# Performance work log

Hardware: AMD Instinct MI355X
Metric: run time of the kernel (lower is better)

## Reference

```python
import jax, jax.numpy as jnp
import numpy as np

SPIRAL_LEN = 12
V_LEVELS = [32768, 8192, 2048, 512, 128]
CHANNELS = [3, 32, 64, 128, 256]


def spiral_conv(x, spiral, W, b):
    # x: [B, V, C_in]; spiral: [V, S] neighbor indices
    B, V, C = x.shape
    g = x[:, spiral, :]                      # [B, V, S, C_in] irregular gather
    g = g.reshape(B, V, -1)                  # [B, V, S*C_in]
    return g @ W + b                         # [B, V, C_out]


def mesh_pool(x, idx, w):
    # sparse down_transform (<=3 nnz per row): out[b,i,:] = sum_k w[i,k] * x[b, idx[i,k], :]
    return jnp.einsum('bvkc,vk->bvc', x[:, idx, :], w)


def setup_inputs() -> dict:
    key = jax.random.key(0)
    ks = jax.random.split(key, 32)
    S = SPIRAL_LEN
    V = V_LEVELS
    C = CHANNELS
    d = {}
    d['x'] = jax.random.normal(ks[0], (32, V[0], C[0]), dtype=jnp.float32)
    for i in range(4):
        d[f'spiral{i}'] = jax.random.randint(ks[1 + i], (V[i], S), 0, V[i])
        d[f'didx{i}'] = jax.random.randint(ks[5 + i], (V[i + 1], 3), 0, V[i])
        w = jax.random.uniform(ks[9 + i], (V[i + 1], 3), dtype=jnp.float32)
        d[f'dw{i}'] = w / w.sum(-1, keepdims=True)  # barycentric-like rows
        fan_in = S * C[i]
        d[f'W{i}'] = jax.random.normal(ks[13 + i], (fan_in, C[i + 1]), dtype=jnp.float32) * np.float32(1.0 / np.sqrt(fan_in))
        d[f'b{i}'] = jnp.zeros((C[i + 1],), jnp.float32)
    flat_in = V[4] * C[4]  # num_vert * out_channels[-2]
    d['Wl1'] = jax.random.normal(ks[20], (flat_in, 512), dtype=jnp.float32) * np.float32(1.0 / np.sqrt(flat_in))
    d['bl1'] = jnp.zeros((512,), jnp.float32)
    d['Wl2'] = jax.random.normal(ks[21], (512, 64), dtype=jnp.float32) * np.float32(1.0 / np.sqrt(512))
    d['bl2'] = jnp.zeros((64,), jnp.float32)
    return d


def reference(x, spiral0, spiral1, spiral2, spiral3,
              didx0, didx1, didx2, didx3,
              dw0, dw1, dw2, dw3,
              W0, b0, W1, b1, W2, b2, W3, b3,
              Wl1, bl1, Wl2, bl2):
    spirals = (spiral0, spiral1, spiral2, spiral3)
    didx = (didx0, didx1, didx2, didx3)
    dw = (dw0, dw1, dw2, dw3)
    Wb = ((W0, b0), (W1, b1), (W2, b2), (W3, b3))
    for i in range(4):  # SpiralEnblock: elu(spiral_conv(x)) -> sparse pool
        x = jax.nn.elu(spiral_conv(x, spirals[i], *Wb[i]))
        x = mesh_pool(x, didx[i], dw[i])
    B = x.shape[0]
    x = x.reshape(B, -1)                     # [B, num_vert * C_last]
    x = jax.nn.elu(x @ Wl1 + bl1)            # [B, 512]
    y = x @ Wl2 + bl2                        # [B, latent]
    return (x, y)
```

## Files before the change

### kernel.cpp

```cpp
#include <hip/hip_runtime.h>
#include <cstdint>
#include <cstddef>

typedef _Float16 f16x8 __attribute__((ext_vector_type(8)));
typedef _Float16 f16x4 __attribute__((ext_vector_type(4)));
typedef float f32x4 __attribute__((ext_vector_type(4)));

static __device__ __forceinline__ float elu_f(float t) {
    return t > 0.0f ? t : expm1f(t);
}

typedef __attribute__((address_space(1))) const unsigned int guint;
typedef __attribute__((address_space(3))) unsigned int       luint;
static __device__ __forceinline__ void gload_lds16(const void* g, void* l)
{
    __builtin_amdgcn_global_load_lds((guint*)g, (luint*)l, 16, 0, 0);
}

template<int N>
static __device__ __forceinline__ void vm_wait()
{
    static_assert(N == 0 || N == 4 || N == 5, "vmcnt literal");
    if constexpr (N == 0)      asm volatile("s_waitcnt vmcnt(0)" ::: "memory");
    else if constexpr (N == 4) asm volatile("s_waitcnt vmcnt(4)" ::: "memory");
    else                       asm volatile("s_waitcnt vmcnt(5)" ::: "memory");
    __builtin_amdgcn_sched_barrier(0);
}

static __device__ __forceinline__ int block_pu0(int bid, int P, int vshift_out, int nbl)
{
    if (nbl < 0) return bid * P;
    int xcd  = bid & 7;
    int slot = bid >> 3;
    int nb   = slot & ((1 << nbl) - 1);
    int tile = slot >> nbl;
    return ((xcd + (nb << 3)) << vshift_out) + tile * P;
}

template<int KTOT, int C_OUT, int BN>
static __device__ __forceinline__ void prep_w_body(const float* __restrict__ W,
                                                   _Float16* __restrict__ o, int i)
{
    constexpr int KT = KTOT/64;
    int j = i & 7;
    int rest = i >> 3;
    int n = rest % BN;
    int kc = (rest / BN) & 7;
    int t = (rest / (BN*8)) % KT;
    int y = rest / (BN*8*KT);
    int k = t*64 + kc*8 + j;
    o[i] = (_Float16)W[(size_t)k*C_OUT + y*BN + n];
}

__global__ __launch_bounds__(256)
void setup_all(const float* __restrict__ x0, _Float16* __restrict__ xT,
               const float* __restrict__ W0, const float* __restrict__ W1,
               const float* __restrict__ W2, const float* __restrict__ W3,
               const int* __restrict__ didx0, const int* __restrict__ spiral0,
               _Float16* __restrict__ w0h, _Float16* __restrict__ w1h,
               _Float16* __restrict__ w2h, _Float16* __restrict__ w3h,
               unsigned int* __restrict__ g)
{
    __shared__ _Float16 t[16][64*4 + 8];
    const int tid = threadIdx.x;
    int bid = blockIdx.x;

    if (bid < 1024) {
        const int h  = bid >> 9;
        const float* x = x0 + (size_t)h*16*98304;
        _Float16* xTh  = xT + (size_t)h*2097152;
        const int v0 = (bid & 511) * 64;
        #pragma unroll
        for (int it = 0; it < 4; ++it) {
            int e = it*256 + tid;
            int b = e >> 6, v = e & 63;
            const float* p = x + ((size_t)b*32768 + v0 + v)*3;
            f16x4 hh;
            hh[0] = (_Float16)p[0]; hh[1] = (_Float16)p[1];
            hh[2] = (_Float16)p[2]; hh[3] = (_Float16)0.f;
            *(f16x4*)&t[b][v*4] = hh;
        }
        __syncthreads();
        #pragma unroll
        for (int it = 0; it < 2; ++it) {
            int e = it*256 + tid;
            int vl = e >> 3, s = e & 7;
            f16x4 a = *(const f16x4*)&t[2*s][vl*4];
            f16x4 b = *(const f16x4*)&t[2*s+1][vl*4];
            f16x8 hh;
            hh[0]=a[0]; hh[1]=a[1]; hh[2]=a[2]; hh[3]=a[3];
            hh[4]=b[0]; hh[5]=b[1]; hh[6]=b[2]; hh[7]=b[3];
            *(f16x8*)&xTh[((size_t)(v0+vl)*16 + s*2)*4] = hh;
        }
        return;
    }
    bid -= 1024;

    if (bid < 8) {
        int i = bid*256 + tid;
        int j = i & 7;
        int n = (i >> 3) & 31;
        int kc = i >> 8;
        int k = kc*8 + j;
        int s = k >> 2, c = k & 3;
        float v = (s < 12 && c < 3) ? W0[(size_t)(s*3 + c)*32 + n] : 0.0f;
        w0h[i] = (_Float16)v;
    } else if (bid < 104) {
        prep_w_body< 384,  64, 64>(W1, w1h, (bid - 8)*256 + tid);
    } else if (bid < 488) {
        prep_w_body< 768, 128, 64>(W2, w2h, (bid - 104)*256 + tid);
    } else if (bid < 2024) {
        prep_w_body<1536, 256, 64>(W3, w3h, (bid - 488)*256 + tid);
    } else {
        int i = (bid - 2024)*256 + tid;
        int q = i & 7;
        int row = i >> 3;
        unsigned int val = 0;
        if (q < 6) {
            int v = didx0[row];
            unsigned int s0 = (unsigned int)spiral0[v*12 + q*2];
            unsigned int s1 = (unsigned int)spiral0[v*12 + q*2 + 1];
            val = s0 | (s1 << 16);
        }
        g[i] = val;
    }
}

__global__ __launch_bounds__(256)
void conv0T(const _Float16* __restrict__ xT0, const unsigned int* __restrict__ gidx,
            const _Float16* __restrict__ Wp, const float* __restrict__ bias,
            const float* __restrict__ dwt, _Float16* __restrict__ out0)
{
    __shared__ _Float16 Ep[4][512];
    const int h = blockIdx.x >> 10;
    const _Float16* xT = xT0 + (size_t)h*2097152;
    _Float16* out = out0 + (size_t)h*16*262144;
    const int tid  = threadIdx.x;
    const int wave = tid >> 6;
    const int lane = tid & 63;
    const int quad = lane >> 4;
    const int l16  = lane & 15;
    const int u0   = (blockIdx.x & 1023) * 8 + wave * 2;

    f16x8 bf[2][2];
    #pragma unroll
    for (int kt = 0; kt < 2; ++kt)
        #pragma unroll
        for (int nt = 0; nt < 2; ++nt)
            bf[kt][nt] = *(const f16x8*)&Wp[(((kt*4+quad)*32) + nt*16 + l16)*8];
    float bv[2] = { bias[l16], bias[16 + l16] };

    #pragma unroll
    for (int ui = 0; ui < 2; ++ui) {
        int u = u0 + ui;
        f32x4 pacc[2] = {{0.f,0.f,0.f,0.f},{0.f,0.f,0.f,0.f}};
        #pragma unroll
        for (int kp = 0; kp < 3; ++kp) {
            int r = u*3 + kp;
            unsigned int gp0 = gidx[r*8 + quad];
            unsigned int gp1 = gidx[r*8 + 4 + quad];
            f16x4 a0 = *(const f16x4*)&xT[(size_t)(gp0 & 0xffffu)*64 + l16*4];
            f16x4 a1 = *(const f16x4*)&xT[(size_t)(gp0 >> 16)*64 + l16*4];
            f16x4 a2 = *(const f16x4*)&xT[(size_t)(gp1 & 0xffffu)*64 + l16*4];
            f16x4 a3 = *(const f16x4*)&xT[(size_t)(gp1 >> 16)*64 + l16*4];
            f16x8 af0, af1;
            af0[0]=a0[0]; af0[1]=a0[1]; af0[2]=a0[2]; af0[3]=a0[3];
            af0[4]=a1[0]; af0[5]=a1[1]; af0[6]=a1[2]; af0[7]=a1[3];
            af1[0]=a2[0]; af1[1]=a2[1]; af1[2]=a2[2]; af1[3]=a2[3];
            af1[4]=a3[0]; af1[5]=a3[1]; af1[6]=a3[2]; af1[7]=a3[3];
            float dw = dwt[r];
            #pragma unroll
            for (int nt = 0; nt < 2; ++nt) {
                f32x4 m = {0.f,0.f,0.f,0.f};
                m = __builtin_amdgcn_mfma_f32_16x16x32_f16(af0, bf[0][nt], m, 0,0,0);
                m = __builtin_amdgcn_mfma_f32_16x16x32_f16(af1, bf[1][nt], m, 0,0,0);
                #pragma unroll
                for (int rr = 0; rr < 4; ++rr)
                    pacc[nt][rr] += dw * elu_f(m[rr] + bv[nt]);
            }
        }
        #pragma unroll
        for (int nt = 0; nt < 2; ++nt)
            #pragma unroll
            for (int rr = 0; rr < 4; ++rr)
                Ep[wave][(quad*4+rr)*32 + nt*16 + l16] = (_Float16)pacc[nt][rr];
        int b  = lane >> 2;
        int c8 = lane & 3;
        f16x8 rowv = *(const f16x8*)&Ep[wave][b*32 + c8*8];
        *(f16x8*)&out[(size_t)b*262144 + (size_t)u*32 + c8*8] = rowv;
    }
}

template<int C_IN, int C_OUT, int P, int BN, int WGM, int WGN, bool OUT_HALF, int NBUF>
__global__ __launch_bounds__(256)
void conv_pool_mfma(const _Float16* __restrict__ x, const int* __restrict__ spiral,
                    const _Float16* __restrict__ Wp, const float* __restrict__ bias,
                    const int* __restrict__ didx, const float* __restrict__ dwt,
                    void* __restrict__ outv, int vshift_in, int vshift_out, int nbl)
{
    constexpr int R    = 3*P;
    constexpr int KTOT = 12*C_IN;
    constexpr int KT   = KTOT/64;
    constexpr int NST  = KT*2;
    constexpr int WTM  = R/WGM;
    constexpr int WTN  = BN/WGN;
    constexpr int NMT  = WTM/16;
    constexpr int NNT  = WTN/16;
    constexpr int C4   = BN/4;
    constexpr int GS   = (C_IN == 32) ? 1 : 2;
    constexpr int NG   = NST / GS;
    constexpr int CPR  = GS * 4;
    constexpr int CPRS = (CPR == 4) ? 2 : 3;
    constexpr int ACH  = R * CPR;
    constexpr int BCH  = GS * BN * 4;
    constexpr int AIPW = ACH / 256;
    constexpr int BIPW = BCH / 256;
    constexpr int LPW  = AIPW + BIPW;
    constexpr int ASUBH = R * GS * 32;
    constexpr int BSUBH = GS * 32 * BN;
    static_assert(WTM % 16 == 0 && WTN % 16 == 0, "tile");
    static_assert(R <= 256 && (P*C4) % 256 == 0, "loops");
    static_assert(ACH % 256 == 0 && BCH % 256 == 0, "stage");
    static_assert(NST % GS == 0 && GS*32 <= C_IN, "group");
    static_assert(NBUF == 2 || NBUF == 3, "nbuf");
    static_assert(NBUF == 2 ? NG >= 2 : NG >= 3, "pipeline depth");

    constexpr size_t BUFB = (size_t)(NBUF*(ASUBH + BSUBH)) * 2;
    constexpr size_t EB   = (size_t)R * (BN + 4) * 2;
    constexpr size_t GOFF = (BUFB > EB ? BUFB : EB);
    static_assert(GOFF + (size_t)R*12*2 <= 65536, "LDS budget");
    __shared__ __align__(16) char smem[GOFF + (size_t)R*12*2];
    _Float16* Ab = (_Float16*)smem;
    _Float16* Bb = (_Float16*)(smem + (size_t)NBUF*ASUBH*2);
    unsigned short* gidx = (unsigned short*)(smem + GOFF);
    _Float16* E = (_Float16*)smem;

    const int tid  = threadIdx.x;
    const int wave = tid >> 6;
    const int lane = tid & 63;
    const int quad = lane >> 4;
    const int l16  = lane & 15;
    const int wm   = wave / WGN;
    const int wn   = wave % WGN;
    const int pu0  = block_pu0(blockIdx.x, P, vshift_out, nbl);
    const int n0   = blockIdx.y * BN;
    const int vmask_out = (1 << vshift_out) - 1;
    const int base_in = (pu0 >> vshift_out) << vshift_in;

    if (tid < R) {
        int ul = tid / 3;
        int kp = tid - ul*3;
        int u  = (pu0 + ul) & vmask_out;
        int v  = didx[u*3 + kp];
        const int* svp = spiral + v*12;
        #pragma unroll
        for (int j = 0; j < 12; ++j) gidx[tid*12 + j] = (unsigned short)svp[j];
    }
    __syncthreads();

    f32x4 acc[NMT][NNT];
    #pragma unroll
    for (int i = 0; i < NMT; ++i)
        #pragma unroll
        for (int j = 0; j < NNT; ++j) acc[i][j] = (f32x4){0.f, 0.f, 0.f, 0.f};

    const _Float16* xb = x + (size_t)base_in * C_IN;

    auto SWZ = [](int r) -> int {
        return (CPR == 4) ? ((r & 3) ^ ((r >> 2) & 3)) : (r & 7);
    };

    auto stage = [&](int g, int buf) {
        const int k0g = g * GS * 32;
        const int sv  = k0g / C_IN;
        const int c0  = k0g % C_IN;
        _Float16* Ad = Ab + (size_t)buf * ASUBH;
        #pragma unroll
        for (int i = 0; i < AIPW; ++i) {
            int t  = (wave*AIPW + i)*64 + lane;
            int r  = t >> CPRS;
            int q  = t & (CPR - 1);
            int qq = q ^ SWZ(r);
            int gr = gidx[r*12 + sv];
            gload_lds16(xb + (size_t)gr*C_IN + c0 + qq*8,
                        Ad + (size_t)(wave*AIPW + i)*512);
        }
        _Float16* Bd = Bb + (size_t)buf * BSUBH;
        const _Float16* bs = Wp + ((size_t)(blockIdx.y*NST + g*GS)*4)*BN*8;
        #pragma unroll
        for (int i = 0; i < BIPW; ++i) {
            int t = (wave*BIPW + i)*64 + lane;
            gload_lds16(bs + (size_t)t*8,
                        Bd + (size_t)(wave*BIPW + i)*512);
        }
    };

    auto compute = [&](int cb) {
        const _Float16* Ar = Ab + (size_t)cb * ASUBH;
        const _Float16* Br = Bb + (size_t)cb * BSUBH;
        #pragma unroll
        for (int sl = 0; sl < GS; ++sl) {
            f16x8 af[NMT], bf[NNT];
            #pragma unroll
            for (int i = 0; i < NMT; ++i) {
                int m = wm*WTM + i*16 + l16;
                af[i] = *(const f16x8*)&Ar[(size_t)(m*CPR + ((sl*4 + quad) ^ SWZ(m)))*8];
            }
            #pragma unroll
            for (int j = 0; j < NNT; ++j) {
                int n = wn*WTN + j*16 + l16;
                bf[j] = *(const f16x8*)&Br[(size_t)((sl*4 + quad)*BN + n)*8];
            }
            #pragma unroll
            for (int i = 0; i < NMT; ++i)
                #pragma unroll
                for (int j = 0; j < NNT; ++j)
                    acc[i][j] = __builtin_amdgcn_mfma_f32_16x16x32_f16(
                        af[i], bf[j], acc[i][j], 0, 0, 0);
        }
    };

    if constexpr (NBUF == 3) {
        stage(0, 0);
        stage(1, 1);
        int cur = 0;
        for (int g = 0; g < NG; ++g) {
            if (g + 1 < NG) vm_wait<LPW>(); else vm_wait<0>();
            __builtin_amdgcn_s_barrier();
            __builtin_amdgcn_sched_barrier(0);
            int nx2 = cur + 2; if (nx2 >= 3) nx2 -= 3;
            if (g + 2 < NG) stage(g + 2, nx2);
            compute(cur);
            asm volatile("s_waitcnt lgkmcnt(0)" ::: "memory");
            __builtin_amdgcn_sched_barrier(0);
            __builtin_amdgcn_s_barrier();
            __builtin_amdgcn_sched_barrier(0);
            cur = (cur + 1 == 3) ? 0 : cur + 1;
        }
    } else {
        stage(0, 0);
        int cur = 0;
        for (int g = 0; g < NG; ++g) {
            if (g + 1 < NG) {
                stage(g + 1, cur ^ 1);
                vm_wait<LPW>();
            } else {
                vm_wait<0>();
            }
            __builtin_amdgcn_s_barrier();
            __builtin_amdgcn_sched_barrier(0);
            compute(cur);
            asm volatile("s_waitcnt lgkmcnt(0)" ::: "memory");
            __builtin_amdgcn_sched_barrier(0);
            __builtin_amdgcn_s_barrier();
            __builtin_amdgcn_sched_barrier(0);
            cur ^= 1;
        }
    }

    float bv[NNT];
    #pragma unroll
    for (int j = 0; j < NNT; ++j)
        bv[j] = bias[n0 + wn*WTN + j*16 + l16];

    #pragma unroll
    for (int i = 0; i < NMT; ++i) {
        int row_base = wm*WTM + i*16 + quad*4;
        #pragma unroll
        for (int j = 0; j < NNT; ++j) {
            int col = wn*WTN + j*16 + l16;
            #pragma unroll
            for (int r = 0; r < 4; ++r)
                E[(size_t)(row_base + r)*(BN+4) + col] =
                    (_Float16)elu_f(acc[i][j][r] + bv[j]);
        }
    }
    __syncthreads();

    #pragma unroll
    for (int e = tid; e < P*C4; e += 256) {
        int ul = e / C4;
        int c4 = e - ul*C4;
        int pu = pu0 + ul;
        int u  = pu & vmask_out;
        const float* w = dwt + u*3;
        f16x4 a0 = *(const f16x4*)&E[(size_t)(ul*3 + 0)*(BN+4) + c4*4];
        f16x4 a1 = *(const f16x4*)&E[(size_t)(ul*3 + 1)*(BN+4) + c4*4];
        f16x4 a2 = *(const f16x4*)&E[(size_t)(ul*3 + 2)*(BN+4) + c4*4];
        float ox = w[0]*(float)a0[0] + w[1]*(float)a1[0] + w[2]*(float)a2[0];
        float oy = w[0]*(float)a0[1] + w[1]*(float)a1[1] + w[2]*(float)a2[1];
        float oz = w[0]*(float)a0[2] + w[1]*(float)a1[2] + w[2]*(float)a2[2];
        float ow = w[0]*(float)a0[3] + w[1]*(float)a1[3] + w[2]*(float)a2[3];
        if (OUT_HALF) {
            f16x4 h; h[0]=(_Float16)ox; h[1]=(_Float16)oy; h[2]=(_Float16)oz; h[3]=(_Float16)ow;
            *(f16x4*)&((_Float16*)outv)[(size_t)pu*C_OUT + n0 + c4*4] = h;
        } else {
            float4 o; o.x=ox; o.y=oy; o.z=oz; o.w=ow;
            *(float4*)&((float*)outv)[(size_t)pu*C_OUT + n0 + c4*4] = o;
        }
    }
}

__global__ __launch_bounds__(256)
void fc1_partial(const float* __restrict__ xflat, const float* __restrict__ Wl1,
                 float* __restrict__ partial)
{
    __shared__ float sb[8704];
    const int tid = threadIdx.x;
    const int n4 = tid & 31;
    const int kq = (tid >> 5) & 3;
    const int mh = tid >> 7;
    const int nt = blockIdx.x;
    const int ks = blockIdx.y;
    const int kbase = ks * 128;

    for (int e = tid; e < 1024; e += 256) {
        int m = e >> 5, k4 = e & 31;
        *(float4*)&sb[m*128 + k4*4] = *(const float4*)&xflat[(size_t)m*32768 + kbase + k4*4];
    }
    __syncthreads();

    float acc[16][4];
    #pragma unroll
    for (int m = 0; m < 16; ++m)
        #pragma unroll
        for (int c = 0; c < 4; ++c) acc[m][c] = 0.0f;

    const float* Wb = Wl1 + (size_t)(kbase + kq*32)*512 + nt*128 + n4*4;
    #pragma unroll 2
    for (int i = 0; i < 32; i += 4) {
        float4 w0 = *(const float4*)(Wb + (size_t)(i+0)*512);
        float4 w1 = *(const float4*)(Wb + (size_t)(i+1)*512);
        float4 w2 = *(const float4*)(Wb + (size_t)(i+2)*512);
        float4 w3 = *(const float4*)(Wb + (size_t)(i+3)*512);
        #pragma unroll
        for (int m = 0; m < 16; ++m) {
            float4 xv = *(const float4*)&sb[(mh*16 + m)*128 + kq*32 + i];
            acc[m][0] += xv.x*w0.x + xv.y*w1.x + xv.z*w2.x + xv.w*w3.x;
            acc[m][1] += xv.x*w0.y + xv.y*w1.y + xv.z*w2.y + xv.w*w3.y;
            acc[m][2] += xv.x*w0.z + xv.y*w1.z + xv.z*w2.z + xv.w*w3.z;
            acc[m][3] += xv.x*w0.w + xv.y*w1.w + xv.z*w2.w + xv.w*w3.w;
        }
    }
    __syncthreads();

    int slot = (mh*2 + (kq >> 1))*32 + n4;
    if (kq & 1) {
        #pragma unroll
        for (int m = 0; m < 16; ++m)
            *(float4*)&sb[slot*68 + m*4] = *(float4*)&acc[m][0];
    }
    __syncthreads();
    if (!(kq & 1)) {
        #pragma unroll
        for (int m = 0; m < 16; ++m) {
            float4 v = *(const float4*)&sb[slot*68 + m*4];
            acc[m][0] += v.x; acc[m][1] += v.y; acc[m][2] += v.z; acc[m][3] += v.w;
        }
    }
    __syncthreads();
    int slot2 = mh*32 + n4;
    if (kq == 2) {
        #pragma unroll
        for (int m = 0; m < 16; ++m)
            *(float4*)&sb[slot2*68 + m*4] = *(float4*)&acc[m][0];
    }
    __syncthreads();
    if (kq == 0) {
        float* pb = partial + ((size_t)(ks*4 + nt)*32 + mh*16)*128 + n4*4;
        #pragma unroll
        for (int m = 0; m < 16; ++m) {
            float4 v = *(const float4*)&sb[slot2*68 + m*4];
            float4 o;
            o.x = acc[m][0] + v.x; o.y = acc[m][1] + v.y;
            o.z = acc[m][2] + v.z; o.w = acc[m][3] + v.w;
            *(float4*)(pb + (size_t)m*128) = o;
        }
    }
}

__global__ __launch_bounds__(512)
void fc1_finish(const float* __restrict__ partial, const float* __restrict__ bl1,
                const float* __restrict__ Wl2, const float* __restrict__ bl2,
                float* __restrict__ out)
{
    __shared__ float hh[512];
    __shared__ float ps[512];
    const int m = blockIdx.x;
    const int tid = threadIdx.x;
    const int nt = tid >> 7, nl = tid & 127;

    const float* p = partial + ((size_t)nt*32 + m)*128 + nl;
    float s = 0.0f;
    #pragma unroll 8
    for (int ks = 0; ks < 256; ++ks)
        s += p[(size_t)ks*16384];
    float h = elu_f(s + bl1[tid]);
    out[(size_t)m*512 + tid] = h;
    hh[tid] = h;
    __syncthreads();

    const int c  = tid & 63;
    const int kc = tid >> 6;
    float a = 0.0f;
    #pragma unroll 8
    for (int k = kc*64; k < kc*64 + 64; ++k)
        a += hh[k] * Wl2[(size_t)k*64 + c];
    ps[tid] = a;
    __syncthreads();
    if (tid < 64) {
        float y = bl2[tid];
        #pragma unroll
        for (int j = 0; j < 8; ++j) y += ps[j*64 + tid];
        out[16384 + (size_t)m*64 + tid] = y;
    }
}

extern "C" void kernel_launch(void* const* d_in, const int* in_sizes, int n_in,
                              void* d_out, int out_size, void* d_ws, size_t ws_size,
                              hipStream_t stream)
{
    (void)in_sizes; (void)n_in; (void)out_size; (void)ws_size;

    const float* x0 = (const float*)d_in[0];
    const int*   sp[4]; const int* didx[4]; const float* dwp[4];
    const float* Wp[4]; const float* bp[4];
    for (int i = 0; i < 4; ++i) {
        sp[i]   = (const int*)  d_in[1 + i*5 + 0];
        didx[i] = (const int*)  d_in[1 + i*5 + 1];
        dwp[i]  = (const float*)d_in[1 + i*5 + 2];
        Wp[i]   = (const float*)d_in[1 + i*5 + 3];
        bp[i]   = (const float*)d_in[1 + i*5 + 4];
    }
    const float* Wl1 = (const float*)d_in[21];
    const float* bl1 = (const float*)d_in[22];
    const float* Wl2 = (const float*)d_in[23];
    const float* bl2 = (const float*)d_in[24];
    float* out = (float*)d_out;

    char* wsb = (char*)d_ws;
    float* persist      = (float*)wsb;
    float* partial      = (float*)(wsb + (4<<20));
    _Float16* xT        = (_Float16*)(wsb + (24<<20));
    _Float16* pooled0   = (_Float16*)(wsb + (32<<20));
    _Float16* pooled1   = (_Float16*)(wsb + (48<<20));
    _Float16* pooled2   = (_Float16*)(wsb + (56<<20));
    unsigned int* gidx0 = (unsigned int*)(wsb + (60<<20));
    _Float16* w0h       = (_Float16*)(wsb + (61<<20));
    _Float16* w1h       = w0h + 2048;
    _Float16* w2h       = w1h + 24576;
    _Float16* w3h       = w2h + 98304;

    setup_all<<<3816, 256, 0, stream>>>(x0, xT,
                                        Wp[0], Wp[1], Wp[2], Wp[3],
                                        didx[0], sp[0],
                                        w0h, w1h, w2h, w3h, gidx0);

    conv0T<<<2048, 256, 0, stream>>>(xT, gidx0, w0h, bp[0], dwp[0], pooled0);

    conv_pool_mfma<32,64,64,64,4,1,true,2><<<1024, 256, 0, stream>>>(
        pooled0, sp[1], w1h, bp[1], didx[1], dwp[1], pooled1, 13, 11, 2);

    conv_pool_mfma<64,128,32,64,2,2,true,3><<<dim3(512, 2), 256, 0, stream>>>(
        pooled1, sp[2], w2h, bp[2], didx[2], dwp[2], pooled2, 11, 9, 2);

    conv_pool_mfma<128,256,32,64,2,2,false,3><<<dim3(128, 4), 256, 0, stream>>>(
        pooled2, sp[3], w3h, bp[3], didx[3], dwp[3], persist, 9, 7, 2);

    fc1_partial<<<dim3(4, 256), 256, 0, stream>>>(persist, Wl1, partial);
    fc1_finish<<<32, 512, 0, stream>>>(partial, bl1, Wl2, bl2, out);
}
```

Measured before the change: 269.2 us.

## Load conv weight fragments directly into registers instead of staging through LDS

Adds a BREG mode to the spiral conv+pool MFMA kernel in which B (weight) fragments are loaded from global memory straight into double-buffered registers, and only the gathered A tile goes through LDS via the triple-buffered global_load_lds path. The main loop is unrolled by two to ping-pong the register buffers, and the vmcnt waits are retuned to cover both A and B loads. This is meant to remove the LDS write/read traffic and footprint for the weights in layers 2 and 3. In exchange each wave issues redundant global loads for B, since the tile is no longer shared through LDS, and register pressure rises.

After: 266.4 us. About the same (-1.1%).

```diff
diff --git a/kernel.cpp b/kernel.cpp
--- a/kernel.cpp
+++ b/kernel.cpp
@@ -20,10 +20,11 @@
 template<int N>
 static __device__ __forceinline__ void vm_wait()
 {
-    static_assert(N == 0 || N == 4 || N == 5, "vmcnt literal");
+    static_assert(N == 0 || N == 4 || N == 5 || N == 7, "vmcnt literal");
     if constexpr (N == 0)      asm volatile("s_waitcnt vmcnt(0)" ::: "memory");
     else if constexpr (N == 4) asm volatile("s_waitcnt vmcnt(4)" ::: "memory");
-    else                       asm volatile("s_waitcnt vmcnt(5)" ::: "memory");
+    else if constexpr (N == 5) asm volatile("s_waitcnt vmcnt(5)" ::: "memory");
+    else                       asm volatile("s_waitcnt vmcnt(7)" ::: "memory");
     __builtin_amdgcn_sched_barrier(0);
 }
 
@@ -191,7 +192,7 @@
     }
 }
 
-template<int C_IN, int C_OUT, int P, int BN, int WGM, int WGN, bool OUT_HALF, int NBUF>
+template<int C_IN, int C_OUT, int P, int BN, int WGM, int WGN, bool OUT_HALF, int NBUF, bool BREG>
 __global__ __launch_bounds__(256)
 void conv_pool_mfma(const _Float16* __restrict__ x, const int* __restrict__ spiral,
                     const _Float16* __restrict__ Wp, const float* __restrict__ bias,
@@ -216,16 +217,21 @@
     constexpr int AIPW = ACH / 256;
     constexpr int BIPW = BCH / 256;
     constexpr int LPW  = AIPW + BIPW;
+    constexpr int NB   = GS * NNT;
+    constexpr int FULLW = AIPW + NB;
     constexpr int ASUBH = R * GS * 32;
     constexpr int BSUBH = GS * 32 * BN;
     static_assert(WTM % 16 == 0 && WTN % 16 == 0, "tile");
     static_assert(R <= 256 && (P*C4) % 256 == 0, "loops");
-    static_assert(ACH % 256 == 0 && BCH % 256 == 0, "stage");
+    static_assert(ACH % 256 == 0, "stageA");
+    static_assert(BREG || BCH % 256 == 0, "stageB");
     static_assert(NST % GS == 0 && GS*32 <= C_IN, "group");
     static_assert(NBUF == 2 || NBUF == 3, "nbuf");
-    static_assert(NBUF == 2 ? NG >= 2 : NG >= 3, "pipeline depth");
-
-    constexpr size_t BUFB = (size_t)(NBUF*(ASUBH + BSUBH)) * 2;
+    static_assert(!BREG || (NBUF == 3 && NG % 2 == 0 && NG >= 4), "breg pipeline");
+    static_assert(BREG || (NBUF == 2 ? NG >= 2 : NG >= 3), "pipeline depth");
+
+    constexpr size_t BUFB = (BREG ? (size_t)NBUF*ASUBH
+                                  : (size_t)NBUF*(ASUBH + BSUBH)) * 2;
     constexpr size_t EB   = (size_t)R * (BN + 4) * 2;
     constexpr size_t GOFF = (BUFB > EB ? BUFB : EB);
     static_assert(GOFF + (size_t)R*12*2 <= 65536, "LDS budget");
@@ -270,7 +276,7 @@
         return (CPR == 4) ? ((r & 3) ^ ((r >> 2) & 3)) : (r & 7);
     };
 
-    auto stage = [&](int g, int buf) {
+    auto stageA = [&](int g, int buf) {
         const int k0g = g * GS * 32;
         const int sv  = k0g / C_IN;
         const int c0  = k0g % C_IN;
@@ -285,76 +291,135 @@
             gload_lds16(xb + (size_t)gr*C_IN + c0 + qq*8,
                         Ad + (size_t)(wave*AIPW + i)*512);
         }
-        _Float16* Bd = Bb + (size_t)buf * BSUBH;
-        const _Float16* bs = Wp + ((size_t)(blockIdx.y*NST + g*GS)*4)*BN*8;
-        #pragma unroll
-        for (int i = 0; i < BIPW; ++i) {
-            int t = (wave*BIPW + i)*64 + lane;
-            gload_lds16(bs + (size_t)t*8,
-                        Bd + (size_t)(wave*BIPW + i)*512);
+        if constexpr (!BREG) {
+            _Float16* Bd = Bb + (size_t)buf * BSUBH;
+            const _Float16* bs = Wp + ((size_t)(blockIdx.y*NST + g*GS)*4)*BN*8;
+            #pragma unroll
+            for (int i = 0; i < BIPW; ++i) {
+                int t = (wave*BIPW + i)*64 + lane;
+                gload_lds16(bs + (size_t)t*8,
+                            Bd + (size_t)(wave*BIPW + i)*512);
+            }
         }
     };
 
-    auto compute = [&](int cb) {
-        const _Float16* Ar = Ab + (size_t)cb * ASUBH;
-        const _Float16* Br = Bb + (size_t)cb * BSUBH;
-        #pragma unroll
-        for (int sl = 0; sl < GS; ++sl) {
-            f16x8 af[NMT], bf[NNT];
+    if constexpr (BREG) {
+        f16x8 b0[GS][NNT], b1[GS][NNT];
+        auto loadB = [&](int g, f16x8 (&br)[GS][NNT]) {
+            const _Float16* bs = Wp + ((size_t)(blockIdx.y*NST + g*GS)*4)*BN*8;
             #pragma unroll
-            for (int i = 0; i < NMT; ++i) {
-                int m = wm*WTM + i*16 + l16;
-                af[i] = *(const f16x8*)&Ar[(size_t)(m*CPR + ((sl*4 + quad) ^ SWZ(m)))*8];
+            for (int sl = 0; sl < GS; ++sl)
+                #pragma unroll
+                for (int j = 0; j < NNT; ++j) {
+                    int n = wn*WTN + j*16 + l16;
+                    br[sl][j] = *(const f16x8*)&bs[(size_t)((sl*4 + quad)*BN + n)*8];
+                }
+        };
+        auto computeR = [&](int cb, f16x8 (&br)[GS][NNT]) {
+            const _Float16* Ar = Ab + (size_t)cb * ASUBH;
+            #pragma unroll
+            for (int sl = 0; sl < GS; ++sl) {
+                f16x8 af[NMT];
+                #pragma unroll
+                for (int i = 0; i < NMT; ++i) {
+                    int m = wm*WTM + i*16 + l16;
+                    af[i] = *(const f16x8*)&Ar[(size_t)(m*CPR + ((sl*4 + quad) ^ SWZ(m)))*8];
+                }
+                #pragma unroll
+                for (int i = 0; i < NMT; ++i)
+                    #pragma unroll
+                    for (int j = 0; j < NNT; ++j)
+                        acc[i][j] = __builtin_amdgcn_mfma_f32_16x16x32_f16(
+                            af[i], br[sl][j], acc[i][j], 0, 0, 0);
             }
-            #pragma unroll
-            for (int j = 0; j < NNT; ++j) {
-                int n = wn*WTN + j*16 + l16;
-                bf[j] = *(const f16x8*)&Br[(size_t)((sl*4 + quad)*BN + n)*8];
-            }
-            #pragma unroll
-            for (int i = 0; i < NMT; ++i)
-                #pragma unroll
-                for (int j = 0; j < NNT; ++j)
-                    acc[i][j] = __builtin_amdgcn_mfma_f32_16x16x32_f16(
-                        af[i], bf[j], acc[i][j], 0, 0, 0);
-        }
-    };
-
-    if constexpr (NBUF == 3) {
-        stage(0, 0);
-        stage(1, 1);
-        int cur = 0;
-        for (int g = 0; g < NG; ++g) {
-            if (g + 1 < NG) vm_wait<LPW>(); else vm_wait<0>();
+        };
+
+        stageA(0, 0);
+        stageA(1, 1);
+        loadB(0, b0);
+        int curA = 0;
+        auto body = [&](int g, f16x8 (&bUse)[GS][NNT], f16x8 (&bFill)[GS][NNT]) {
+            int nx2 = curA + 2; if (nx2 >= 3) nx2 -= 3;
+            if (g + 2 < NG) stageA(g + 2, nx2);
+            if (g + 1 < NG) loadB(g + 1, bFill);
+            __builtin_amdgcn_sched_barrier(0);
+            if (g + 2 < NG)      vm_wait<FULLW>();
+            else if (g + 1 < NG) vm_wait<NB>();
+            else                 vm_wait<0>();
             __builtin_amdgcn_s_barrier();
             __builtin_amdgcn_sched_barrier(0);
-            int nx2 = cur + 2; if (nx2 >= 3) nx2 -= 3;
-            if (g + 2 < NG) stage(g + 2, nx2);
-            compute(cur);
+            computeR(curA, bUse);
             asm volatile("s_waitcnt lgkmcnt(0)" ::: "memory");
             __builtin_amdgcn_sched_barrier(0);
             __builtin_amdgcn_s_barrier();
             __builtin_amdgcn_sched_barrier(0);
-            cur = (cur + 1 == 3) ? 0 : cur + 1;
+            curA = (curA + 1 == 3) ? 0 : curA + 1;
+        };
+        for (int g = 0; g < NG; g += 2) {
+            body(g, b0, b1);
+            body(g + 1, b1, b0);
         }
     } else {
-        stage(0, 0);
-        int cur = 0;
-        for (int g = 0; g < NG; ++g) {
-            if (g + 1 < NG) {
-                stage(g + 1, cur ^ 1);
-                vm_wait<LPW>();
-            } else {
-                vm_wait<0>();
+        auto compute = [&](int cb) {
+            const _Float16* Ar = Ab + (size_t)cb * ASUBH;
+            const _Float16* Br = Bb + (size_t)cb * BSUBH;
+            #pragma unroll
+            for (int sl = 0; sl < GS; ++sl) {
+                f16x8 af[NMT], bf[NNT];
+                #pragma unroll
+                for (int i = 0; i < NMT; ++i) {
+                    int m = wm*WTM + i*16 + l16;
+                    af[i] = *(const f16x8*)&Ar[(size_t)(m*CPR + ((sl*4 + quad) ^ SWZ(m)))*8];
+                }
+                #pragma unroll
+                for (int j = 0; j < NNT; ++j) {
+                    int n = wn*WTN + j*16 + l16;
+                    bf[j] = *(const f16x8*)&Br[(size_t)((sl*4 + quad)*BN + n)*8];
+                }
+                #pragma unroll
+                for (int i = 0; i < NMT; ++i)
+                    #pragma unroll
+                    for (int j = 0; j < NNT; ++j)
+                        acc[i][j] = __builtin_amdgcn_mfma_f32_16x16x32_f16(
+                            af[i], bf[j], acc[i][j], 0, 0, 0);
             }
-            __builtin_amdgcn_s_barrier();
-            __builtin_amdgcn_sched_barrier(0);
-            compute(cur);
-            asm volatile("s_waitcnt lgkmcnt(0)" ::: "memory");
-            __builtin_amdgcn_sched_barrier(0);
-            __builtin_amdgcn_s_barrier();
-            __builtin_amdgcn_sched_barrier(0);
-            cur ^= 1;
+        };
+        if constexpr (NBUF == 3) {
+            stageA(0, 0);
+            stageA(1, 1);
+            int cur = 0;
+            for (int g = 0; g < NG; ++g) {
+                if (g + 1 < NG) vm_wait<LPW>(); else vm_wait<0>();
+                __builtin_amdgcn_s_barrier();
+                __builtin_amdgcn_sched_barrier(0);
+                int nx2 = cur + 2; if (nx2 >= 3) nx2 -= 3;
+                if (g + 2 < NG) stageA(g + 2, nx2);
+                compute(cur);
+                asm volatile("s_waitcnt lgkmcnt(0)" ::: "memory");
+                __builtin_amdgcn_sched_barrier(0);
+                __builtin_amdgcn_s_barrier();
+                __builtin_amdgcn_sched_barrier(0);
+                cur = (cur + 1 == 3) ? 0 : cur + 1;
+            }
+        } else {
+            stageA(0, 0);
+            int cur = 0;
+            for (int g = 0; g < NG; ++g) {
+                if (g + 1 < NG) {
+                    stageA(g + 1, cur ^ 1);
+                    vm_wait<LPW>();
+                } else {
+                    vm_wait<0>();
+                }
+                __builtin_amdgcn_s_barrier();
+                __builtin_amdgcn_sched_barrier(0);
+                compute(cur);
+                asm volatile("s_waitcnt lgkmcnt(0)" ::: "memory");
+                __builtin_amdgcn_sched_barrier(0);
+                __builtin_amdgcn_s_barrier();
+                __builtin_amdgcn_sched_barrier(0);
+                cur ^= 1;
+            }
         }
     }
 
@@ -558,13 +623,13 @@
 
     conv0T<<<2048, 256, 0, stream>>>(xT, gidx0, w0h, bp[0], dwp[0], pooled0);
 
-    conv_pool_mfma<32,64,64,64,4,1,true,2><<<1024, 256, 0, stream>>>(
+    conv_pool_mfma<32,64,64,64,4,1,true,2,false><<<1024, 256, 0, stream>>>(
         pooled0, sp[1], w1h, bp[1], didx[1], dwp[1], pooled1, 13, 11, 2);
 
-    conv_pool_mfma<64,128,32,64,2,2,true,3><<<dim3(512, 2), 256, 0, stream>>>(
+    conv_pool_mfma<64,128,32,64,2,2,true,3,true><<<dim3(512, 2), 256, 0, stream>>>(
         pooled1, sp[2], w2h, bp[2], didx[2], dwp[2], pooled2, 11, 9, 2);
 
-    conv_pool_mfma<128,256,32,64,2,2,false,3><<<dim3(128, 4), 256, 0, stream>>>(
+    conv_pool_mfma<128,256,32,64,2,2,false,3,true><<<dim3(128, 4), 256, 0, stream>>>(
         pooled2, sp[3], w3h, bp[3], didx[3], dwp[3], persist, 9, 7, 2);
 
     fc1_partial<<<dim3(4, 256), 256, 0, stream>>>(persist, Wl1, partial);
```
